# Kernel tuning notes

Measured on AMD Instinct MI355X. Metric: run time of the kernel, lower is better.

## Reference

```python
import jax, jax.numpy as jnp
import numpy as np

N_QUBITS = 13
DEPTH = 4
DIM = 2 ** N_QUBITS
PI = 3.141592653589793

# qubit 0 = most significant bit of the basis-state index
_idx = np.arange(DIM)
BITS = np.stack([(_idx >> (N_QUBITS - 1 - q)) & 1 for q in range(N_QUBITS)], axis=1)  # (DIM, n)
SIGNS = jnp.asarray(1.0 - 2.0 * BITS, dtype=jnp.float32)                               # Z eigenvalues, (DIM, n)
PARITY = jnp.asarray((-1.0) ** BITS.sum(axis=1), dtype=jnp.float32)                    # <Z^{(x)n}> diagonal, (DIM,)
# CZ entangling chain (q, q+1): diagonal (-1)^{sum_q b_q b_{q+1}}
ENT = jnp.asarray((-1.0) ** (BITS[:, :-1] * BITS[:, 1:]).sum(axis=1), dtype=jnp.float32)


def fwht(psi):
    """Normalized fast Walsh-Hadamard transform (H on every qubit), psi: (B, DIM) complex."""
    B = psi.shape[0]
    for q in range(N_QUBITS):
        psi = psi.reshape(B, 2 ** q, 2, -1)
        psi = jnp.stack([psi[:, :, 0] + psi[:, :, 1], psi[:, :, 0] - psi[:, :, 1]], axis=2)
    return psi.reshape(B, DIM) * (2.0 ** (-N_QUBITS / 2))


def feature_map_state(x):
    """Havlicek ZZ feature map: psi = D(x) H^n D(x) H^n |0...0>.
    Diagonal phase per basis state b: sum_j x_j s_j(b) + sum_{j<k} (pi-x_j)(pi-x_k) s_j(b) s_k(b)."""
    a = PI - x                                              # (B, n)
    u = x @ SIGNS.T                                         # (B, DIM)
    v = a @ SIGNS.T                                         # (B, DIM)
    phi = u + 0.5 * (v * v - jnp.sum(a * a, axis=1, keepdims=True))  # pair term via (sum)^2 trick
    d = jnp.exp(1j * phi)                                   # complex64 diagonal
    psi = jnp.full((x.shape[0], DIM), DIM ** -0.5, dtype=jnp.complex64)  # H^n |0>
    psi = fwht(d * psi)
    return d * psi


def _apply_1q(psi, U, q):
    """Apply 2x2 complex gate U to qubit q (bit-sliced)."""
    B = psi.shape[0]
    psi = psi.reshape(B, 2 ** q, 2, -1)
    a0, a1 = psi[:, :, 0], psi[:, :, 1]
    out = jnp.stack([U[0, 0] * a0 + U[0, 1] * a1, U[1, 0] * a0 + U[1, 1] * a1], axis=2)
    return out.reshape(B, DIM)


def variational_apply(psi, theta):
    """(DEPTH+1) layers of per-qubit Rz(b)Ry(a), CZ-chain entanglers between layers."""
    th = theta.reshape(DEPTH + 1, N_QUBITS, 2)
    for l in range(DEPTH + 1):
        if l > 0:
            psi = psi * ENT
        for q in range(N_QUBITS):
            ca = jnp.cos(0.5 * th[l, q, 0])
            sa = jnp.sin(0.5 * th[l, q, 0])
            em = jnp.exp(-0.5j * th[l, q, 1])
            ep = jnp.exp(0.5j * th[l, q, 1])
            U = jnp.stack([jnp.stack([em * ca, -em * sa]), jnp.stack([ep * sa, ep * ca])])
            psi = _apply_1q(psi, U, q)
    return psi


def setup_inputs() -> dict:
    key = jax.random.key(0)
    k1, k2 = jax.random.split(key)
    x = jax.random.normal(k1, (512, N_QUBITS), dtype=jnp.float32)
    theta = 0.1 * jax.random.normal(k2, ((DEPTH + 1) * N_QUBITS * 2,), dtype=jnp.float32)
    bias = jnp.zeros((1,), dtype=jnp.float32)
    return {"x": x, "theta": theta, "bias": bias}


def reference(x, theta, bias):
    psi = feature_map_state(x)
    psi = variational_apply(psi, theta)
    prob = psi.real ** 2 + psi.imag ** 2              # (B, DIM)
    logit = prob @ PARITY + bias[0]                   # (B,)
    return jnp.stack([-logit, logit], axis=1)         # two-class logits
```

## Files before the change

kernel.cpp:

```cpp
#include <hip/hip_runtime.h>
#include <hip/hip_fp16.h>

#define NQ   13
#define DIM  8192
#define PI_F 3.14159265358979323846f
#define NT   256
#define NAMP 32

#define NSLOT 9216

__device__ __forceinline__ int baseH(int t) { return 36 * t; }
__device__ __forceinline__ int baseL(int t) {
  int c = ((t & 1) << 7) | ((t & 2) << 5) | (t >> 2);
  return c + 4 * (c >> 5);
}

union F4H { float4 f; __half2 h[4]; };

__device__ __forceinline__ void rsincos(float x, float* s, float* c) {
  const float INV2PI = 0.15915494309189535f;
  const float TWOPI  = 6.283185307179586f;
  float r = x * INV2PI;
  r -= rintf(r);
  float ang = r * TWOPI;
  *s = __sinf(ang);
  *c = __cosf(ang);
}

__device__ __forceinline__ float2 f2add(float2 a, float2 b) {
  return make_float2(a.x + b.x, a.y + b.y);
}
__device__ __forceinline__ float2 f2sub(float2 a, float2 b) {
  return make_float2(a.x - b.x, a.y - b.y);
}
__device__ __forceinline__ float2 cphase(float2 v, float cs, float sn) {
  return make_float2(fmaf(cs, v.x, -sn * v.y), fmaf(cs, v.y, sn * v.x));
}
__device__ __forceinline__ float2 cmul(float2 a, float2 b) {
  return make_float2(fmaf(a.x, b.x, -a.y * b.y), fmaf(a.x, b.y, a.y * b.x));
}

template<int MASK>
__device__ __forceinline__ __half2 xorLaneH(__half2 v) {
  union { __half2 h; int i; } u, r; u.h = v;
  if constexpr (MASK == 1)
    r.i = __builtin_amdgcn_update_dpp(u.i, u.i, 0xB1, 0xF, 0xF, false);
  else
    r.i = __builtin_amdgcn_update_dpp(u.i, u.i, 0x4E, 0xF, 0xF, false);
  return r.h;
}

__device__ __forceinline__ void loadHh(const __half2* __restrict__ sAmp, int t, __half2* amp) {
  const __half2* p = sAmp + baseH(t);
  #pragma unroll
  for (int k = 0; k < 8; k++) {
    F4H u; u.f = *reinterpret_cast<const float4*>(p + 4 * k);
    #pragma unroll
    for (int c = 0; c < 4; c++) amp[4 * k + c] = u.h[c];
  }
}
__device__ __forceinline__ void storeHh(__half2* __restrict__ sAmp, int t, const __half2* amp) {
  __half2* p = sAmp + baseH(t);
  #pragma unroll
  for (int k = 0; k < 8; k++) {
    F4H u;
    #pragma unroll
    for (int c = 0; c < 4; c++) u.h[c] = amp[4 * k + c];
    *reinterpret_cast<float4*>(p + 4 * k) = u.f;
  }
}
__device__ __forceinline__ void loadLh(const __half2* __restrict__ sAmp, int t, __half2* amp) {
  const __half2* p = sAmp + baseL(t);
  #pragma unroll
  for (int j = 0; j < NAMP; j++) amp[j] = p[288 * j];
}
__device__ __forceinline__ void storeLh(__half2* __restrict__ sAmp, int t, const __half2* amp) {
  __half2* p = sAmp + baseL(t);
  #pragma unroll
  for (int j = 0; j < NAMP; j++) p[288 * j] = amp[j];
}

template<int KB>
__device__ __forceinline__ void fwht_bit(float2* amp) {
  #pragma unroll
  for (int j = 0; j < NAMP; j++) if (!(j & (1 << KB))) {
    int j1 = j | (1 << KB);
    float2 a0 = amp[j], a1 = amp[j1];
    amp[j]  = f2add(a0, a1);
    amp[j1] = f2sub(a0, a1);
  }
}
template<int KB>
__device__ __forceinline__ void fwht_bitH(__half2* amp) {
  #pragma unroll
  for (int j = 0; j < NAMP; j++) if (!(j & (1 << KB))) {
    int j1 = j | (1 << KB);
    __half2 a0 = amp[j], a1 = amp[j1];
    amp[j]  = __hadd2(a0, a1);
    amp[j1] = __hsub2(a0, a1);
  }
}
template<int KB>
__device__ __forceinline__ void applyRyH(__half2* amp, __half2 nta, __half2 sa) {
  #pragma unroll
  for (int j = 0; j < NAMP; j++) if (!(j & (1 << KB))) {
    int j1 = j | (1 << KB);
    amp[j]  = __hfma2(nta, amp[j1], amp[j]);
    amp[j1] = __hfma2(sa,  amp[j],  amp[j1]);
    amp[j]  = __hfma2(nta, amp[j1], amp[j]);
  }
}
template<int MASK>
__device__ __forceinline__ void laneRyH(__half2* amp, __half2 c2, __half2 spm) {
  #pragma unroll
  for (int j = 0; j < NAMP; j++) {
    __half2 p = xorLaneH<MASK>(amp[j]);
    amp[j] = __hfma2(spm, p, __hmul2(c2, amp[j]));
  }
}
template<int MASK>
__device__ __forceinline__ void laneFwhtH(__half2* amp, __half2 sgn) {
  #pragma unroll
  for (int j = 0; j < NAMP; j++) {
    __half2 p = xorLaneH<MASK>(amp[j]);
    amp[j] = __hfma2(sgn, amp[j], p);
  }
}

template<int PAT>
__device__ __forceinline__ void buildTree(const float* __restrict__ w, float bias,
                                          int t, float* s) {
  float base = bias;
  if constexpr (PAT == 0) {
    #pragma unroll
    for (int k = 0; k < 8; k++) base += ((t >> k) & 1) ? w[5 + k] : 0.0f;
  } else {
    constexpr int BM[8] = {7, 6, 0, 1, 2, 3, 4, 5};
    #pragma unroll
    for (int k = 0; k < 8; k++) base += ((t >> k) & 1) ? w[BM[k]] : 0.0f;
  }
  s[0] = base;
  #pragma unroll
  for (int k = 0; k < 5; k++) {
    float wp = w[(PAT == 0) ? k : 8 + k];
    #pragma unroll
    for (int m = 0; m < (1 << k); m++) s[m | (1 << k)] = s[m] + wp;
  }
}

template<int PAT, bool INIT>
__device__ __forceinline__ void featureDiag(float2* amp,
                                            const float* __restrict__ wXp,
                                            const float* __restrict__ wAp,
                                            const float* __restrict__ consp, int t) {
  float u[NAMP], v[NAMP];
  buildTree<PAT>(wXp, consp[0], t, u);
  buildTree<PAT>(wAp, consp[1], t, v);
  float A2 = consp[2];
  #pragma unroll
  for (int j = 0; j < NAMP; j++) {
    float phi = u[j] + 0.5f * (v[j] * v[j] - A2);
    float sn, cs; rsincos(phi, &sn, &cs);
    if constexpr (INIT) amp[j] = make_float2(cs, sn);
    else                amp[j] = cphase(amp[j], cs, sn);
  }
}

__device__ __forceinline__ void applyDiagH(float2* amp,
                                           const float* __restrict__ wb,
                                           const float* __restrict__ eR,
                                           const float* __restrict__ eI,
                                           float bias, int t) {
  float base = bias;
  #pragma unroll
  for (int k = 0; k < 8; k++) base += ((t >> k) & 1) ? wb[5 + k] : 0.0f;
  float2 c[16];
  { float sn, cs; rsincos(base, &sn, &cs);
    float sg = (__popc(t & (t >> 1)) & 1) ? -1.0f : 1.0f;
    c[0] = make_float2(cs * sg, sn * sg); }
  #pragma unroll
  for (int k = 0; k < 4; k++) {
    float2 ep = make_float2(eR[k], eI[k]);
    float2 em = make_float2(-ep.x, -ep.y);
    #pragma unroll
    for (int m = 0; m < (1 << k); m++) {
      bool neg = (k >= 1) && ((m >> (k - 1)) & 1);
      c[m | (1 << k)] = cmul(c[m], neg ? em : ep);
    }
  }
  #pragma unroll
  for (int j = 0; j < 16; j++) amp[j] = cphase(amp[j], c[j].x, c[j].y);
  float2 e4 = make_float2(eR[4], eI[4]);
  if (t & 1) { e4.x = -e4.x; e4.y = -e4.y; }
  float2 e4m = make_float2(-e4.x, -e4.y);
  #pragma unroll
  for (int j = 16; j < 32; j++) {
    float2 cc = cmul(c[j - 16], ((j >> 3) & 1) ? e4m : e4);
    amp[j] = cphase(amp[j], cc.x, cc.y);
  }
}

__device__ __forceinline__ void applyDiagL(float2* amp,
                                           const float* __restrict__ wb,
                                           const float* __restrict__ eR,
                                           const float* __restrict__ eI,
                                           float bias, int t) {
  constexpr int BM[8] = {7, 6, 0, 1, 2, 3, 4, 5};
  float base = bias;
  #pragma unroll
  for (int k = 0; k < 8; k++) base += ((t >> k) & 1) ? wb[BM[k]] : 0.0f;
  const int ci = ((t & 1) << 7) | ((t & 2) << 5) | (t >> 2);
  float2 c[16];
  { float sn, cs; rsincos(base, &sn, &cs);
    float sg = (__popc(ci & (ci >> 1)) & 1) ? -1.0f : 1.0f;
    c[0] = make_float2(cs * sg, sn * sg); }
  {
    float2 e0 = make_float2(eR[8], eI[8]);
    if (t & 1) { e0.x = -e0.x; e0.y = -e0.y; }
    c[1] = cmul(c[0], e0);
  }
  #pragma unroll
  for (int k = 1; k < 4; k++) {
    float2 ep = make_float2(eR[8 + k], eI[8 + k]);
    float2 em = make_float2(-ep.x, -ep.y);
    #pragma unroll
    for (int m = 0; m < (1 << k); m++)
      c[m | (1 << k)] = cmul(c[m], ((m >> (k - 1)) & 1) ? em : ep);
  }
  #pragma unroll
  for (int j = 0; j < 16; j++) amp[j] = cphase(amp[j], c[j].x, c[j].y);
  float2 e4 = make_float2(eR[12], eI[12]);
  float2 e4m = make_float2(-e4.x, -e4.y);
  #pragma unroll
  for (int j = 16; j < 32; j++) {
    float2 cc = cmul(c[j - 16], ((j >> 3) & 1) ? e4m : e4);
    amp[j] = cphase(amp[j], cc.x, cc.y);
  }
}

__device__ __forceinline__ void gatesH(__half2* ampH,
                                       const __half2* __restrict__ hNTA,
                                       const __half2* __restrict__ hSA,
                                       const __half2* __restrict__ hC2,
                                       const __half2* __restrict__ hS2,
                                       int g0, int lane) {
  { __half2 s2 = hS2[g0 + 7]; laneRyH<1>(ampH, hC2[g0 + 7], (lane & 1) ? s2 : __hneg2(s2)); }
  { __half2 s2 = hS2[g0 + 6]; laneRyH<2>(ampH, hC2[g0 + 6], (lane & 2) ? s2 : __hneg2(s2)); }
  applyRyH<0>(ampH, hNTA[g0 + 12], hSA[g0 + 12]);
  applyRyH<1>(ampH, hNTA[g0 + 11], hSA[g0 + 11]);
  applyRyH<2>(ampH, hNTA[g0 + 10], hSA[g0 + 10]);
  applyRyH<3>(ampH, hNTA[g0 + 9],  hSA[g0 + 9]);
  applyRyH<4>(ampH, hNTA[g0 + 8],  hSA[g0 + 8]);
}
__device__ __forceinline__ void gatesL(__half2* ampH,
                                       const __half2* __restrict__ hNTA,
                                       const __half2* __restrict__ hSA,
                                       const __half2* __restrict__ hC2,
                                       const __half2* __restrict__ hS2,
                                       int g0, int lane) {
  { __half2 s2 = hS2[g0 + 5]; laneRyH<1>(ampH, hC2[g0 + 5], (lane & 1) ? s2 : __hneg2(s2)); }
  applyRyH<0>(ampH, hNTA[g0 + 4], hSA[g0 + 4]);
  applyRyH<1>(ampH, hNTA[g0 + 3], hSA[g0 + 3]);
  applyRyH<2>(ampH, hNTA[g0 + 2], hSA[g0 + 2]);
  applyRyH<3>(ampH, hNTA[g0 + 1], hSA[g0 + 1]);
  applyRyH<4>(ampH, hNTA[g0 + 0], hSA[g0 + 0]);
}

__global__ __launch_bounds__(NT, 1) void qc_kernel(
    const float* __restrict__ xin,
    const float* __restrict__ thin,
    const float* __restrict__ bin,
    float* __restrict__ out) {
  __shared__ alignas(16) __half2 sAmp[NSLOT];
  __shared__ __half2 hNTA[65], hSA[65];
  __shared__ __half2 hC2[65], hS2[65];
  __shared__ float gBbit[65];
  __shared__ float eBr[65], eBi[65];
  __shared__ float wX[13], wA[13];
  __shared__ float cons[8];
  __shared__ float red[NT / 64];

  const int t = threadIdx.x;
  const int lane = t & 63;
  const int b = blockIdx.x;

  if (t < NQ) {
    float xq = xin[b * NQ + t];
    float aq = PI_F - xq;
    wX[12 - t] = -2.0f * xq;
    wA[12 - t] = -2.0f * aq;
  }
  if (t < 65) {
    float av = thin[2 * t];
    float bv = thin[2 * t + 1];
    float ca = cosf(0.5f * av);
    float sa = sinf(0.5f * av);
    float ta = sa / (1.0f + ca);
    hNTA[t] = __float2half2_rn(-ta);
    hSA[t]  = __float2half2_rn(sa);
    hC2[t]  = __float2half2_rn(ca);
    hS2[t]  = __float2half2_rn(sa);
    int l = t / NQ, q = t % NQ;
    int s = l * NQ + (12 - q);
    gBbit[s] = bv;
    eBr[s] = cosf(bv);
    eBi[s] = sinf(bv);
  }
  __syncthreads();
  if (t == 0) {
    float X = 0.f, A = 0.f, A2 = 0.f;
    for (int p = 0; p < NQ; p++) {
      float xq = -0.5f * wX[p], aq = -0.5f * wA[p];
      X += xq; A += aq; A2 += aq * aq;
    }
    cons[0] = X; cons[1] = A; cons[2] = A2;
    for (int l = 0; l < 5; l++) {
      float s = 0.f;
      for (int p = 0; p < NQ; p++) s += gBbit[l * NQ + p];
      cons[3 + l] = -0.5f * s;
    }
  }
  __syncthreads();

  const __half2 P1 = __float2half2_rn(1.0f), M1 = __float2half2_rn(-1.0f);

  {
    float2 ampF[NAMP];
    featureDiag<0, true>(ampF, wX, wA, cons, t);
    fwht_bit<0>(ampF); fwht_bit<1>(ampF); fwht_bit<2>(ampF);
    fwht_bit<3>(ampF); fwht_bit<4>(ampF);
    __half2 ampH[NAMP];
    #pragma unroll
    for (int j = 0; j < NAMP; j++) ampH[j] = __float22half2_rn(ampF[j]);
    laneFwhtH<1>(ampH, (lane & 1) ? M1 : P1);
    laneFwhtH<2>(ampH, (lane & 2) ? M1 : P1);
    storeHh(sAmp, t, ampH);
  }
  __syncthreads();

  {
    __half2 ampH[NAMP];
    loadLh(sAmp, t, ampH);
    laneFwhtH<1>(ampH, (lane & 1) ? M1 : P1);
    fwht_bitH<0>(ampH); fwht_bitH<1>(ampH); fwht_bitH<2>(ampH);
    fwht_bitH<3>(ampH); fwht_bitH<4>(ampH);
    float2 ampF[NAMP];
    #pragma unroll
    for (int j = 0; j < NAMP; j++) ampF[j] = __half22float2(ampH[j]);
    featureDiag<1, false>(ampF, wX, wA, cons, t);
    #pragma unroll
    for (int j = 0; j < NAMP; j++) ampH[j] = __float22half2_rn(ampF[j]);
    gatesL(ampH, hNTA, hSA, hC2, hS2, 0, lane);
    storeLh(sAmp, t, ampH);
  }
  __syncthreads();

  for (int l = 0; l < 4; l += 2) {
    const int ga = l * NQ, gb = ga + NQ, gc = gb + NQ;
    {
      __half2 ampH[NAMP];
      loadHh(sAmp, t, ampH);
      gatesH(ampH, hNTA, hSA, hC2, hS2, ga, lane);
      float2 ampF[NAMP];
      #pragma unroll
      for (int j = 0; j < NAMP; j++) ampF[j] = __half22float2(ampH[j]);
      applyDiagH(ampF, gBbit + ga, eBr + ga, eBi + ga, cons[3 + l], t);
      #pragma unroll
      for (int j = 0; j < NAMP; j++) ampH[j] = __float22half2_rn(ampF[j]);
      gatesH(ampH, hNTA, hSA, hC2, hS2, gb, lane);
      storeHh(sAmp, t, ampH);
    }
    __syncthreads();
    {
      __half2 ampH[NAMP];
      loadLh(sAmp, t, ampH);
      gatesL(ampH, hNTA, hSA, hC2, hS2, gb, lane);
      float2 ampF[NAMP];
      #pragma unroll
      for (int j = 0; j < NAMP; j++) ampF[j] = __half22float2(ampH[j]);
      applyDiagL(ampF, gBbit + gb, eBr + gb, eBi + gb, cons[3 + l + 1], t);
      #pragma unroll
      for (int j = 0; j < NAMP; j++) ampH[j] = __float22half2_rn(ampF[j]);
      gatesL(ampH, hNTA, hSA, hC2, hS2, gc, lane);
      storeLh(sAmp, t, ampH);
    }
    __syncthreads();
  }

  float acc = 0.0f;
  {
    const int ga = 4 * NQ;
    __half2 ampH[NAMP];
    loadHh(sAmp, t, ampH);
    gatesH(ampH, hNTA, hSA, hC2, hS2, ga, lane);
    int pt = __popc(t) & 1;
    #pragma unroll
    for (int j = 0; j < NAMP; j++) {
      float2 a = __half22float2(ampH[j]);
      float p2 = fmaf(a.x, a.x, a.y * a.y);
      acc += ((pt + __popc(j)) & 1) ? -p2 : p2;
    }
  }

  #pragma unroll
  for (int off = 32; off > 0; off >>= 1) acc += __shfl_down(acc, off, 64);
  if ((t & 63) == 0) red[t >> 6] = acc;
  __syncthreads();
  if (t == 0) {
    float total = red[0] + red[1] + red[2] + red[3];
    float logit = total * (1.0f / 67108864.0f) + bin[0];
    out[b * 2 + 0] = -logit;
    out[b * 2 + 1] = logit;
  }
}

extern "C" void kernel_launch(void* const* d_in, const int* in_sizes, int n_in,
                              void* d_out, int out_size, void* d_ws, size_t ws_size,
                              hipStream_t stream) {
  const float* x  = (const float*)d_in[0];
  const float* th = (const float*)d_in[1];
  const float* bi = (const float*)d_in[2];
  float* out = (float*)d_out;
  int B = in_sizes[0] / NQ;
  qc_kernel<<<B, NT, 0, stream>>>(x, th, bi, out);
}
```

Baseline: 88.41 us.

## Keep state in registers with lane shuffles and pairwise wave exchanges instead of transposes

Replaces the alternating high/low shared-memory transposes with a fixed layout. Each thread keeps 32 amplitudes in registers, lane-level qubits are handled with DPP or shfl_xor, and the two wave-level qubits are handled by pairwise exchanges through shared memory. Diagonal phases are now computed on half2 amplitudes with per-element float conversion. This removes the strided transposed shared-memory loads, but it adds more syncthreads per layer (two exchanges each with two barriers) and uses ds_swizzle/shfl for the masks 4, 16 and 32.

```diff
diff --git a/kernel.cpp b/kernel.cpp
--- a/kernel.cpp
+++ b/kernel.cpp
@@ -7,13 +7,8 @@
 #define NT   256
 #define NAMP 32
 
+__device__ __forceinline__ int base0(int t) { return 36 * t; }
 #define NSLOT 9216
-
-__device__ __forceinline__ int baseH(int t) { return 36 * t; }
-__device__ __forceinline__ int baseL(int t) {
-  int c = ((t & 1) << 7) | ((t & 2) << 5) | (t >> 2);
-  return c + 4 * (c >> 5);
-}
 
 union F4H { float4 f; __half2 h[4]; };
 
@@ -27,12 +22,6 @@
   *c = __cosf(ang);
 }
 
-__device__ __forceinline__ float2 f2add(float2 a, float2 b) {
-  return make_float2(a.x + b.x, a.y + b.y);
-}
-__device__ __forceinline__ float2 f2sub(float2 a, float2 b) {
-  return make_float2(a.x - b.x, a.y - b.y);
-}
 __device__ __forceinline__ float2 cphase(float2 v, float cs, float sn) {
   return make_float2(fmaf(cs, v.x, -sn * v.y), fmaf(cs, v.y, sn * v.x));
 }
@@ -41,17 +30,21 @@
 }
 
 template<int MASK>
-__device__ __forceinline__ __half2 xorLaneH(__half2 v) {
+__device__ __forceinline__ __half2 lanePartner(__half2 v) {
   union { __half2 h; int i; } u, r; u.h = v;
   if constexpr (MASK == 1)
     r.i = __builtin_amdgcn_update_dpp(u.i, u.i, 0xB1, 0xF, 0xF, false);
+  else if constexpr (MASK == 2)
+    r.i = __builtin_amdgcn_update_dpp(u.i, u.i, 0x4E, 0xF, 0xF, false);
+  else if constexpr (MASK == 8)
+    r.i = __builtin_amdgcn_update_dpp(u.i, u.i, 0x128, 0xF, 0xF, false);
   else
-    r.i = __builtin_amdgcn_update_dpp(u.i, u.i, 0x4E, 0xF, 0xF, false);
+    r.i = __shfl_xor(u.i, MASK, 64);
   return r.h;
 }
 
-__device__ __forceinline__ void loadHh(const __half2* __restrict__ sAmp, int t, __half2* amp) {
-  const __half2* p = sAmp + baseH(t);
+__device__ __forceinline__ void loadXh(const __half2* __restrict__ sAmp, int t, __half2* amp) {
+  const __half2* p = sAmp + base0(t);
   #pragma unroll
   for (int k = 0; k < 8; k++) {
     F4H u; u.f = *reinterpret_cast<const float4*>(p + 4 * k);
@@ -59,8 +52,8 @@
     for (int c = 0; c < 4; c++) amp[4 * k + c] = u.h[c];
   }
 }
-__device__ __forceinline__ void storeHh(__half2* __restrict__ sAmp, int t, const __half2* amp) {
-  __half2* p = sAmp + baseH(t);
+__device__ __forceinline__ void storeXh(__half2* __restrict__ sAmp, int t, const __half2* amp) {
+  __half2* p = sAmp + base0(t);
   #pragma unroll
   for (int k = 0; k < 8; k++) {
     F4H u;
@@ -69,27 +62,7 @@
     *reinterpret_cast<float4*>(p + 4 * k) = u.f;
   }
 }
-__device__ __forceinline__ void loadLh(const __half2* __restrict__ sAmp, int t, __half2* amp) {
-  const __half2* p = sAmp + baseL(t);
-  #pragma unroll
-  for (int j = 0; j < NAMP; j++) amp[j] = p[288 * j];
-}
-__device__ __forceinline__ void storeLh(__half2* __restrict__ sAmp, int t, const __half2* amp) {
-  __half2* p = sAmp + baseL(t);
-  #pragma unroll
-  for (int j = 0; j < NAMP; j++) p[288 * j] = amp[j];
-}
-
-template<int KB>
-__device__ __forceinline__ void fwht_bit(float2* amp) {
-  #pragma unroll
-  for (int j = 0; j < NAMP; j++) if (!(j & (1 << KB))) {
-    int j1 = j | (1 << KB);
-    float2 a0 = amp[j], a1 = amp[j1];
-    amp[j]  = f2add(a0, a1);
-    amp[j1] = f2sub(a0, a1);
-  }
-}
+
 template<int KB>
 __device__ __forceinline__ void fwht_bitH(__half2* amp) {
   #pragma unroll
@@ -114,7 +87,7 @@
 __device__ __forceinline__ void laneRyH(__half2* amp, __half2 c2, __half2 spm) {
   #pragma unroll
   for (int j = 0; j < NAMP; j++) {
-    __half2 p = xorLaneH<MASK>(amp[j]);
+    __half2 p = lanePartner<MASK>(amp[j]);
     amp[j] = __hfma2(spm, p, __hmul2(c2, amp[j]));
   }
 }
@@ -122,103 +95,67 @@
 __device__ __forceinline__ void laneFwhtH(__half2* amp, __half2 sgn) {
   #pragma unroll
   for (int j = 0; j < NAMP; j++) {
-    __half2 p = xorLaneH<MASK>(amp[j]);
+    __half2 p = lanePartner<MASK>(amp[j]);
     amp[j] = __hfma2(sgn, amp[j], p);
   }
 }
 
-template<int PAT>
-__device__ __forceinline__ void buildTree(const float* __restrict__ w, float bias,
-                                          int t, float* s) {
-  float base = bias;
-  if constexpr (PAT == 0) {
-    #pragma unroll
-    for (int k = 0; k < 8; k++) base += ((t >> k) & 1) ? w[5 + k] : 0.0f;
-  } else {
-    constexpr int BM[8] = {7, 6, 0, 1, 2, 3, 4, 5};
-    #pragma unroll
-    for (int k = 0; k < 8; k++) base += ((t >> k) & 1) ? w[BM[k]] : 0.0f;
-  }
-  s[0] = base;
-  #pragma unroll
-  for (int k = 0; k < 5; k++) {
-    float wp = w[(PAT == 0) ? k : 8 + k];
-    #pragma unroll
-    for (int m = 0; m < (1 << k); m++) s[m | (1 << k)] = s[m] + wp;
-  }
-}
-
-template<int PAT, bool INIT>
-__device__ __forceinline__ void featureDiag(float2* amp,
+template<bool INIT>
+__device__ __forceinline__ void featureDiag(__half2* amp,
                                             const float* __restrict__ wXp,
                                             const float* __restrict__ wAp,
-                                            const float* __restrict__ consp, int t) {
-  float u[NAMP], v[NAMP];
-  buildTree<PAT>(wXp, consp[0], t, u);
-  buildTree<PAT>(wAp, consp[1], t, v);
-  float A2 = consp[2];
+                                            const float* __restrict__ consp,
+                                            int tl, int w0, int w1) {
+  float u16[16], v16[16];
+  float ub = consp[0], vb = consp[1];
+  #pragma unroll
+  for (int k = 0; k < 6; k++) if ((tl >> k) & 1) { ub += wXp[k]; vb += wAp[k]; }
+  if (w0) { ub += wXp[6]; vb += wAp[6]; }
+  if (w1) { ub += wXp[7]; vb += wAp[7]; }
+  u16[0] = ub; v16[0] = vb;
+  #pragma unroll
+  for (int k = 0; k < 4; k++) {
+    float wu = wXp[8 + k], wv = wAp[8 + k];
+    #pragma unroll
+    for (int m = 0; m < (1 << k); m++) {
+      u16[m | (1 << k)] = u16[m] + wu;
+      v16[m | (1 << k)] = v16[m] + wv;
+    }
+  }
+  const float du = wXp[12], dv = wAp[12], A2 = consp[2];
   #pragma unroll
   for (int j = 0; j < NAMP; j++) {
-    float phi = u[j] + 0.5f * (v[j] * v[j] - A2);
+    float uu = u16[j & 15] + ((j >> 4) ? du : 0.0f);
+    float vv = v16[j & 15] + ((j >> 4) ? dv : 0.0f);
+    float phi = uu + 0.5f * (vv * vv - A2);
     float sn, cs; rsincos(phi, &sn, &cs);
-    if constexpr (INIT) amp[j] = make_float2(cs, sn);
-    else                amp[j] = cphase(amp[j], cs, sn);
-  }
-}
-
-__device__ __forceinline__ void applyDiagH(float2* amp,
-                                           const float* __restrict__ wb,
-                                           const float* __restrict__ eR,
-                                           const float* __restrict__ eI,
-                                           float bias, int t) {
+    if constexpr (INIT) {
+      amp[j] = __float22half2_rn(make_float2(cs, sn));
+    } else {
+      float2 a = __half22float2(amp[j]);
+      amp[j] = __float22half2_rn(cphase(a, cs, sn));
+    }
+  }
+}
+
+__device__ __forceinline__ void applyDiag(__half2* amp,
+                                          const float* __restrict__ wb,
+                                          const float* __restrict__ eR,
+                                          const float* __restrict__ eI,
+                                          float bias, int tl, int w0, int w1) {
   float base = bias;
   #pragma unroll
-  for (int k = 0; k < 8; k++) base += ((t >> k) & 1) ? wb[5 + k] : 0.0f;
+  for (int k = 0; k < 6; k++) if ((tl >> k) & 1) base += wb[k];
+  if (w0) base += wb[6];
+  if (w1) base += wb[7];
   float2 c[16];
   { float sn, cs; rsincos(base, &sn, &cs);
-    float sg = (__popc(t & (t >> 1)) & 1) ? -1.0f : 1.0f;
-    c[0] = make_float2(cs * sg, sn * sg); }
-  #pragma unroll
-  for (int k = 0; k < 4; k++) {
-    float2 ep = make_float2(eR[k], eI[k]);
-    float2 em = make_float2(-ep.x, -ep.y);
-    #pragma unroll
-    for (int m = 0; m < (1 << k); m++) {
-      bool neg = (k >= 1) && ((m >> (k - 1)) & 1);
-      c[m | (1 << k)] = cmul(c[m], neg ? em : ep);
-    }
-  }
-  #pragma unroll
-  for (int j = 0; j < 16; j++) amp[j] = cphase(amp[j], c[j].x, c[j].y);
-  float2 e4 = make_float2(eR[4], eI[4]);
-  if (t & 1) { e4.x = -e4.x; e4.y = -e4.y; }
-  float2 e4m = make_float2(-e4.x, -e4.y);
-  #pragma unroll
-  for (int j = 16; j < 32; j++) {
-    float2 cc = cmul(c[j - 16], ((j >> 3) & 1) ? e4m : e4);
-    amp[j] = cphase(amp[j], cc.x, cc.y);
-  }
-}
-
-__device__ __forceinline__ void applyDiagL(float2* amp,
-                                           const float* __restrict__ wb,
-                                           const float* __restrict__ eR,
-                                           const float* __restrict__ eI,
-                                           float bias, int t) {
-  constexpr int BM[8] = {7, 6, 0, 1, 2, 3, 4, 5};
-  float base = bias;
-  #pragma unroll
-  for (int k = 0; k < 8; k++) base += ((t >> k) & 1) ? wb[BM[k]] : 0.0f;
-  const int ci = ((t & 1) << 7) | ((t & 2) << 5) | (t >> 2);
-  float2 c[16];
-  { float sn, cs; rsincos(base, &sn, &cs);
-    float sg = (__popc(ci & (ci >> 1)) & 1) ? -1.0f : 1.0f;
-    c[0] = make_float2(cs * sg, sn * sg); }
-  {
-    float2 e0 = make_float2(eR[8], eI[8]);
-    if (t & 1) { e0.x = -e0.x; e0.y = -e0.y; }
-    c[1] = cmul(c[0], e0);
-  }
+    int sg = (__popc(tl & (tl >> 1)) ^ (((tl >> 5) & 1) & w0) ^ (w0 & w1)) & 1;
+    float s = sg ? -1.0f : 1.0f;
+    c[0] = make_float2(cs * s, sn * s); }
+  { float2 e0 = make_float2(eR[8], eI[8]);
+    if (w1) { e0.x = -e0.x; e0.y = -e0.y; }
+    c[1] = cmul(c[0], e0); }
   #pragma unroll
   for (int k = 1; k < 4; k++) {
     float2 ep = make_float2(eR[8 + k], eI[8 + k]);
@@ -228,42 +165,18 @@
       c[m | (1 << k)] = cmul(c[m], ((m >> (k - 1)) & 1) ? em : ep);
   }
   #pragma unroll
-  for (int j = 0; j < 16; j++) amp[j] = cphase(amp[j], c[j].x, c[j].y);
-  float2 e4 = make_float2(eR[12], eI[12]);
+  for (int j = 0; j < 16; j++) {
+    float2 a = __half22float2(amp[j]);
+    amp[j] = __float22half2_rn(cphase(a, c[j].x, c[j].y));
+  }
+  float2 e4  = make_float2(eR[12], eI[12]);
   float2 e4m = make_float2(-e4.x, -e4.y);
   #pragma unroll
   for (int j = 16; j < 32; j++) {
-    float2 cc = cmul(c[j - 16], ((j >> 3) & 1) ? e4m : e4);
-    amp[j] = cphase(amp[j], cc.x, cc.y);
-  }
-}
-
-__device__ __forceinline__ void gatesH(__half2* ampH,
-                                       const __half2* __restrict__ hNTA,
-                                       const __half2* __restrict__ hSA,
-                                       const __half2* __restrict__ hC2,
-                                       const __half2* __restrict__ hS2,
-                                       int g0, int lane) {
-  { __half2 s2 = hS2[g0 + 7]; laneRyH<1>(ampH, hC2[g0 + 7], (lane & 1) ? s2 : __hneg2(s2)); }
-  { __half2 s2 = hS2[g0 + 6]; laneRyH<2>(ampH, hC2[g0 + 6], (lane & 2) ? s2 : __hneg2(s2)); }
-  applyRyH<0>(ampH, hNTA[g0 + 12], hSA[g0 + 12]);
-  applyRyH<1>(ampH, hNTA[g0 + 11], hSA[g0 + 11]);
-  applyRyH<2>(ampH, hNTA[g0 + 10], hSA[g0 + 10]);
-  applyRyH<3>(ampH, hNTA[g0 + 9],  hSA[g0 + 9]);
-  applyRyH<4>(ampH, hNTA[g0 + 8],  hSA[g0 + 8]);
-}
-__device__ __forceinline__ void gatesL(__half2* ampH,
-                                       const __half2* __restrict__ hNTA,
-                                       const __half2* __restrict__ hSA,
-                                       const __half2* __restrict__ hC2,
-                                       const __half2* __restrict__ hS2,
-                                       int g0, int lane) {
-  { __half2 s2 = hS2[g0 + 5]; laneRyH<1>(ampH, hC2[g0 + 5], (lane & 1) ? s2 : __hneg2(s2)); }
-  applyRyH<0>(ampH, hNTA[g0 + 4], hSA[g0 + 4]);
-  applyRyH<1>(ampH, hNTA[g0 + 3], hSA[g0 + 3]);
-  applyRyH<2>(ampH, hNTA[g0 + 2], hSA[g0 + 2]);
-  applyRyH<3>(ampH, hNTA[g0 + 1], hSA[g0 + 1]);
-  applyRyH<4>(ampH, hNTA[g0 + 0], hSA[g0 + 0]);
+    float2 cc = cmul(c[j - 16], (((j - 16) >> 3) & 1) ? e4m : e4);
+    float2 a = __half22float2(amp[j]);
+    amp[j] = __float22half2_rn(cphase(a, cc.x, cc.y));
+  }
 }
 
 __global__ __launch_bounds__(NT, 1) void qc_kernel(
@@ -271,7 +184,7 @@
     const float* __restrict__ thin,
     const float* __restrict__ bin,
     float* __restrict__ out) {
-  __shared__ alignas(16) __half2 sAmp[NSLOT];
+  __shared__ alignas(16) __half2 sEx[NSLOT];
   __shared__ __half2 hNTA[65], hSA[65];
   __shared__ __half2 hC2[65], hS2[65];
   __shared__ float gBbit[65];
@@ -280,9 +193,11 @@
   __shared__ float cons[8];
   __shared__ float red[NT / 64];
 
-  const int t = threadIdx.x;
-  const int lane = t & 63;
-  const int b = blockIdx.x;
+  const int t  = threadIdx.x;
+  const int tl = t & 63;
+  const int w0 = (t >> 6) & 1;
+  const int w1 = (t >> 7) & 1;
+  const int b  = blockIdx.x;
 
   if (t < NQ) {
     float xq = xin[b * NQ + t];
@@ -322,83 +237,75 @@
   }
   __syncthreads();
 
+  __half2 amp[NAMP];
   const __half2 P1 = __float2half2_rn(1.0f), M1 = __float2half2_rn(-1.0f);
 
-  {
-    float2 ampF[NAMP];
-    featureDiag<0, true>(ampF, wX, wA, cons, t);
-    fwht_bit<0>(ampF); fwht_bit<1>(ampF); fwht_bit<2>(ampF);
-    fwht_bit<3>(ampF); fwht_bit<4>(ampF);
-    __half2 ampH[NAMP];
-    #pragma unroll
-    for (int j = 0; j < NAMP; j++) ampH[j] = __float22half2_rn(ampF[j]);
-    laneFwhtH<1>(ampH, (lane & 1) ? M1 : P1);
-    laneFwhtH<2>(ampH, (lane & 2) ? M1 : P1);
-    storeHh(sAmp, t, ampH);
-  }
-  __syncthreads();
-
-  {
-    __half2 ampH[NAMP];
-    loadLh(sAmp, t, ampH);
-    laneFwhtH<1>(ampH, (lane & 1) ? M1 : P1);
-    fwht_bitH<0>(ampH); fwht_bitH<1>(ampH); fwht_bitH<2>(ampH);
-    fwht_bitH<3>(ampH); fwht_bitH<4>(ampH);
-    float2 ampF[NAMP];
-    #pragma unroll
-    for (int j = 0; j < NAMP; j++) ampF[j] = __half22float2(ampH[j]);
-    featureDiag<1, false>(ampF, wX, wA, cons, t);
-    #pragma unroll
-    for (int j = 0; j < NAMP; j++) ampH[j] = __float22half2_rn(ampF[j]);
-    gatesL(ampH, hNTA, hSA, hC2, hS2, 0, lane);
-    storeLh(sAmp, t, ampH);
-  }
-  __syncthreads();
-
-  for (int l = 0; l < 4; l += 2) {
-    const int ga = l * NQ, gb = ga + NQ, gc = gb + NQ;
-    {
-      __half2 ampH[NAMP];
-      loadHh(sAmp, t, ampH);
-      gatesH(ampH, hNTA, hSA, hC2, hS2, ga, lane);
-      float2 ampF[NAMP];
+  auto exchFwht = [&](int bit) {
+    __syncthreads();
+    storeXh(sEx, t, amp);
+    __syncthreads();
+    __half2 p[NAMP];
+    loadXh(sEx, t ^ (64 << bit), p);
+    int wb = bit ? w1 : w0;
+    __half2 sgn = wb ? M1 : P1;
+    #pragma unroll
+    for (int j = 0; j < NAMP; j++) amp[j] = __hfma2(sgn, amp[j], p[j]);
+  };
+  auto exchRy = [&](int bit, int gq) {
+    __syncthreads();
+    storeXh(sEx, t, amp);
+    __syncthreads();
+    __half2 p[NAMP];
+    loadXh(sEx, t ^ (64 << bit), p);
+    int wb = bit ? w1 : w0;
+    __half2 c2 = hC2[gq], s2 = hS2[gq];
+    __half2 spm = wb ? s2 : __hneg2(s2);
+    #pragma unroll
+    for (int j = 0; j < NAMP; j++)
+      amp[j] = __hfma2(spm, p[j], __hmul2(c2, amp[j]));
+  };
+
+  featureDiag<true>(amp, wX, wA, cons, tl, w0, w1);
+
+  fwht_bitH<0>(amp); fwht_bitH<1>(amp); fwht_bitH<2>(amp);
+  fwht_bitH<3>(amp); fwht_bitH<4>(amp);
+  laneFwhtH<1>(amp,  (tl & 1)  ? M1 : P1);
+  laneFwhtH<2>(amp,  (tl & 2)  ? M1 : P1);
+  laneFwhtH<4>(amp,  (tl & 4)  ? M1 : P1);
+  laneFwhtH<8>(amp,  (tl & 8)  ? M1 : P1);
+  laneFwhtH<16>(amp, (tl & 16) ? M1 : P1);
+  laneFwhtH<32>(amp, (tl & 32) ? M1 : P1);
+  exchFwht(0);
+  exchFwht(1);
+
+  featureDiag<false>(amp, wX, wA, cons, tl, w0, w1);
+
+  float acc = 0.0f;
+  for (int l = 0; l < 5; ++l) {
+    const int g = l * NQ;
+    applyRyH<4>(amp, hNTA[g + 0], hSA[g + 0]);
+    applyRyH<3>(amp, hNTA[g + 1], hSA[g + 1]);
+    applyRyH<2>(amp, hNTA[g + 2], hSA[g + 2]);
+    applyRyH<1>(amp, hNTA[g + 3], hSA[g + 3]);
+    applyRyH<0>(amp, hNTA[g + 4], hSA[g + 4]);
+    { __half2 s2 = hS2[g + 12]; laneRyH<1>(amp,  hC2[g + 12], (tl & 1)  ? s2 : __hneg2(s2)); }
+    { __half2 s2 = hS2[g + 11]; laneRyH<2>(amp,  hC2[g + 11], (tl & 2)  ? s2 : __hneg2(s2)); }
+    { __half2 s2 = hS2[g + 10]; laneRyH<4>(amp,  hC2[g + 10], (tl & 4)  ? s2 : __hneg2(s2)); }
+    { __half2 s2 = hS2[g + 9];  laneRyH<8>(amp,  hC2[g + 9],  (tl & 8)  ? s2 : __hneg2(s2)); }
+    { __half2 s2 = hS2[g + 8];  laneRyH<16>(amp, hC2[g + 8],  (tl & 16) ? s2 : __hneg2(s2)); }
+    { __half2 s2 = hS2[g + 7];  laneRyH<32>(amp, hC2[g + 7],  (tl & 32) ? s2 : __hneg2(s2)); }
+    exchRy(0, g + 6);
+    exchRy(1, g + 5);
+    if (l < 4) {
+      applyDiag(amp, gBbit + g, eBr + g, eBi + g, cons[3 + l], tl, w0, w1);
+    } else {
+      int pt = __popc(t) & 1;
       #pragma unroll
-      for (int j = 0; j < NAMP; j++) ampF[j] = __half22float2(ampH[j]);
-      applyDiagH(ampF, gBbit + ga, eBr + ga, eBi + ga, cons[3 + l], t);
-      #pragma unroll
-      for (int j = 0; j < NAMP; j++) ampH[j] = __float22half2_rn(ampF[j]);
-      gatesH(ampH, hNTA, hSA, hC2, hS2, gb, lane);
-      storeHh(sAmp, t, ampH);
-    }
-    __syncthreads();
-    {
-      __half2 ampH[NAMP];
-      loadLh(sAmp, t, ampH);
-      gatesL(ampH, hNTA, hSA, hC2, hS2, gb, lane);
-      float2 ampF[NAMP];
-      #pragma unroll
-      for (int j = 0; j < NAMP; j++) ampF[j] = __half22float2(ampH[j]);
-      applyDiagL(ampF, gBbit + gb, eBr + gb, eBi + gb, cons[3 + l + 1], t);
-      #pragma unroll
-      for (int j = 0; j < NAMP; j++) ampH[j] = __float22half2_rn(ampF[j]);
-      gatesL(ampH, hNTA, hSA, hC2, hS2, gc, lane);
-      storeLh(sAmp, t, ampH);
-    }
-    __syncthreads();
-  }
-
-  float acc = 0.0f;
-  {
-    const int ga = 4 * NQ;
-    __half2 ampH[NAMP];
-    loadHh(sAmp, t, ampH);
-    gatesH(ampH, hNTA, hSA, hC2, hS2, ga, lane);
-    int pt = __popc(t) & 1;
-    #pragma unroll
-    for (int j = 0; j < NAMP; j++) {
-      float2 a = __half22float2(ampH[j]);
-      float p2 = fmaf(a.x, a.x, a.y * a.y);
-      acc += ((pt + __popc(j)) & 1) ? -p2 : p2;
+      for (int j = 0; j < NAMP; j++) {
+        float2 a = __half22float2(amp[j]);
+        float p2 = fmaf(a.x, a.x, a.y * a.y);
+        acc += ((pt + __popc(j)) & 1) ? -p2 : p2;
+      }
     }
   }
 
```

Result: slower. 98.81 us (+11.8%).

## Remap the second-phase shared-memory layout to vectorized column loads with extra lane shuffles

Applied to the files above, without the earlier changes.

The qubit-to-register/lane mapping for the second (L/C) phase is changed so each thread loads 4 consecutive half2 amplitudes with float4 accesses (8 vector loads) instead of 32 scalar strided loads. To make this work, more qubits are handled through cross-lane exchanges: DPP row_ror for mask 8 and __shfl_xor for masks 4 and 16 in the first FWHT stage, plus an extra lane Ry in the H phase. The feature and entangler diagonal generators are rewritten for the new bit mapping. The aim is to cut LDS instruction count and bank-conflict cost, in exchange for extra cross-lane shuffle work (ds_bpermute for the non-DPP masks).

```diff
diff --git a/kernel.cpp b/kernel.cpp
--- a/kernel.cpp
+++ b/kernel.cpp
@@ -6,13 +6,12 @@
 #define PI_F 3.14159265358979323846f
 #define NT   256
 #define NAMP 32
-
 #define NSLOT 9216
 
 __device__ __forceinline__ int baseH(int t) { return 36 * t; }
-__device__ __forceinline__ int baseL(int t) {
-  int c = ((t & 1) << 7) | ((t & 2) << 5) | (t >> 2);
-  return c + 4 * (c >> 5);
+__device__ __forceinline__ int fC(int t) {
+  return ((t & 1) << 7) | (((t >> 1) & 1) << 9) | (((t >> 2) & 0x1F) << 2)
+       | (((t >> 7) & 1) << 8);
 }
 
 union F4H { float4 f; __half2 h[4]; };
@@ -41,12 +40,16 @@
 }
 
 template<int MASK>
-__device__ __forceinline__ __half2 xorLaneH(__half2 v) {
+__device__ __forceinline__ __half2 lanePartner(__half2 v) {
   union { __half2 h; int i; } u, r; u.h = v;
   if constexpr (MASK == 1)
     r.i = __builtin_amdgcn_update_dpp(u.i, u.i, 0xB1, 0xF, 0xF, false);
+  else if constexpr (MASK == 2)
+    r.i = __builtin_amdgcn_update_dpp(u.i, u.i, 0x4E, 0xF, 0xF, false);
+  else if constexpr (MASK == 8)
+    r.i = __builtin_amdgcn_update_dpp(u.i, u.i, 0x128, 0xF, 0xF, false);
   else
-    r.i = __builtin_amdgcn_update_dpp(u.i, u.i, 0x4E, 0xF, 0xF, false);
+    r.i = __shfl_xor(u.i, MASK, 64);
   return r.h;
 }
 
@@ -69,15 +72,24 @@
     *reinterpret_cast<float4*>(p + 4 * k) = u.f;
   }
 }
-__device__ __forceinline__ void loadLh(const __half2* __restrict__ sAmp, int t, __half2* amp) {
-  const __half2* p = sAmp + baseL(t);
-  #pragma unroll
-  for (int j = 0; j < NAMP; j++) amp[j] = p[288 * j];
-}
-__device__ __forceinline__ void storeLh(__half2* __restrict__ sAmp, int t, const __half2* amp) {
-  __half2* p = sAmp + baseL(t);
-  #pragma unroll
-  for (int j = 0; j < NAMP; j++) p[288 * j] = amp[j];
+__device__ __forceinline__ void loadCh(const __half2* __restrict__ sAmp, int cpad, __half2* amp) {
+  const __half2* p = sAmp + cpad;
+  #pragma unroll
+  for (int g = 0; g < 8; g++) {
+    F4H u; u.f = *reinterpret_cast<const float4*>(p + 1152 * g);
+    #pragma unroll
+    for (int c = 0; c < 4; c++) amp[4 * g + c] = u.h[c];
+  }
+}
+__device__ __forceinline__ void storeCh(__half2* __restrict__ sAmp, int cpad, const __half2* amp) {
+  __half2* p = sAmp + cpad;
+  #pragma unroll
+  for (int g = 0; g < 8; g++) {
+    F4H u;
+    #pragma unroll
+    for (int c = 0; c < 4; c++) u.h[c] = amp[4 * g + c];
+    *reinterpret_cast<float4*>(p + 1152 * g) = u.f;
+  }
 }
 
 template<int KB>
@@ -114,7 +126,7 @@
 __device__ __forceinline__ void laneRyH(__half2* amp, __half2 c2, __half2 spm) {
   #pragma unroll
   for (int j = 0; j < NAMP; j++) {
-    __half2 p = xorLaneH<MASK>(amp[j]);
+    __half2 p = lanePartner<MASK>(amp[j]);
     amp[j] = __hfma2(spm, p, __hmul2(c2, amp[j]));
   }
 }
@@ -122,40 +134,30 @@
 __device__ __forceinline__ void laneFwhtH(__half2* amp, __half2 sgn) {
   #pragma unroll
   for (int j = 0; j < NAMP; j++) {
-    __half2 p = xorLaneH<MASK>(amp[j]);
+    __half2 p = lanePartner<MASK>(amp[j]);
     amp[j] = __hfma2(sgn, amp[j], p);
   }
 }
 
-template<int PAT>
-__device__ __forceinline__ void buildTree(const float* __restrict__ w, float bias,
-                                          int t, float* s) {
-  float base = bias;
-  if constexpr (PAT == 0) {
-    #pragma unroll
-    for (int k = 0; k < 8; k++) base += ((t >> k) & 1) ? w[5 + k] : 0.0f;
-  } else {
-    constexpr int BM[8] = {7, 6, 0, 1, 2, 3, 4, 5};
-    #pragma unroll
-    for (int k = 0; k < 8; k++) base += ((t >> k) & 1) ? w[BM[k]] : 0.0f;
-  }
-  s[0] = base;
+template<bool INIT>
+__device__ __forceinline__ void featureDiagH(float2* amp,
+                                             const float* __restrict__ wXp,
+                                             const float* __restrict__ wAp,
+                                             const float* __restrict__ consp, int t) {
+  float u[NAMP], v[NAMP];
+  float ub = consp[0], vb = consp[1];
+  #pragma unroll
+  for (int k = 0; k < 8; k++) if ((t >> k) & 1) { ub += wXp[5 + k]; vb += wAp[5 + k]; }
+  u[0] = ub; v[0] = vb;
   #pragma unroll
   for (int k = 0; k < 5; k++) {
-    float wp = w[(PAT == 0) ? k : 8 + k];
-    #pragma unroll
-    for (int m = 0; m < (1 << k); m++) s[m | (1 << k)] = s[m] + wp;
-  }
-}
-
-template<int PAT, bool INIT>
-__device__ __forceinline__ void featureDiag(float2* amp,
-                                            const float* __restrict__ wXp,
-                                            const float* __restrict__ wAp,
-                                            const float* __restrict__ consp, int t) {
-  float u[NAMP], v[NAMP];
-  buildTree<PAT>(wXp, consp[0], t, u);
-  buildTree<PAT>(wAp, consp[1], t, v);
+    float wu = wXp[k], wv = wAp[k];
+    #pragma unroll
+    for (int m = 0; m < (1 << k); m++) {
+      u[m | (1 << k)] = u[m] + wu;
+      v[m | (1 << k)] = v[m] + wv;
+    }
+  }
   float A2 = consp[2];
   #pragma unroll
   for (int j = 0; j < NAMP; j++) {
@@ -163,6 +165,34 @@
     float sn, cs; rsincos(phi, &sn, &cs);
     if constexpr (INIT) amp[j] = make_float2(cs, sn);
     else                amp[j] = cphase(amp[j], cs, sn);
+  }
+}
+
+__device__ __forceinline__ void featureDiagC(float2* amp,
+                                             const float* __restrict__ wXp,
+                                             const float* __restrict__ wAp,
+                                             const float* __restrict__ consp, int ic) {
+  float u[NAMP], v[NAMP];
+  float ub = consp[0], vb = consp[1];
+  #pragma unroll
+  for (int k = 2; k <= 9; k++) if ((ic >> k) & 1) { ub += wXp[k]; vb += wAp[k]; }
+  u[0] = ub; v[0] = vb;
+  constexpr int P[5] = {0, 1, 10, 11, 12};
+  #pragma unroll
+  for (int k = 0; k < 5; k++) {
+    float wu = wXp[P[k]], wv = wAp[P[k]];
+    #pragma unroll
+    for (int m = 0; m < (1 << k); m++) {
+      u[m | (1 << k)] = u[m] + wu;
+      v[m | (1 << k)] = v[m] + wv;
+    }
+  }
+  float A2 = consp[2];
+  #pragma unroll
+  for (int j = 0; j < NAMP; j++) {
+    float phi = u[j] + 0.5f * (v[j] * v[j] - A2);
+    float sn, cs; rsincos(phi, &sn, &cs);
+    amp[j] = cphase(amp[j], cs, sn);
   }
 }
 
@@ -200,36 +230,37 @@
   }
 }
 
-__device__ __forceinline__ void applyDiagL(float2* amp,
+__device__ __forceinline__ void applyDiagC(float2* amp,
                                            const float* __restrict__ wb,
                                            const float* __restrict__ eR,
                                            const float* __restrict__ eI,
-                                           float bias, int t) {
-  constexpr int BM[8] = {7, 6, 0, 1, 2, 3, 4, 5};
+                                           float bias, int ic) {
   float base = bias;
   #pragma unroll
-  for (int k = 0; k < 8; k++) base += ((t >> k) & 1) ? wb[BM[k]] : 0.0f;
-  const int ci = ((t & 1) << 7) | ((t & 2) << 5) | (t >> 2);
+  for (int k = 2; k <= 9; k++) base += ((ic >> k) & 1) ? wb[k] : 0.0f;
   float2 c[16];
   { float sn, cs; rsincos(base, &sn, &cs);
-    float sg = (__popc(ci & (ci >> 1)) & 1) ? -1.0f : 1.0f;
+    float sg = (__popc(ic & (ic >> 1)) & 1) ? -1.0f : 1.0f;
     c[0] = make_float2(cs * sg, sn * sg); }
-  {
-    float2 e0 = make_float2(eR[8], eI[8]);
-    if (t & 1) { e0.x = -e0.x; e0.y = -e0.y; }
-    c[1] = cmul(c[0], e0);
-  }
-  #pragma unroll
-  for (int k = 1; k < 4; k++) {
-    float2 ep = make_float2(eR[8 + k], eI[8 + k]);
-    float2 em = make_float2(-ep.x, -ep.y);
-    #pragma unroll
-    for (int m = 0; m < (1 << k); m++)
-      c[m | (1 << k)] = cmul(c[m], ((m >> (k - 1)) & 1) ? em : ep);
-  }
+  { float2 e0 = make_float2(eR[0], eI[0]);
+    c[1] = cmul(c[0], e0); }
+  { float2 e1 = make_float2(eR[1], eI[1]);
+    if ((ic >> 2) & 1) { e1.x = -e1.x; e1.y = -e1.y; }
+    float2 e1m = make_float2(-e1.x, -e1.y);
+    c[2] = cmul(c[0], e1);
+    c[3] = cmul(c[1], e1m); }
+  { float2 e2 = make_float2(eR[10], eI[10]);
+    if ((ic >> 9) & 1) { e2.x = -e2.x; e2.y = -e2.y; }
+    #pragma unroll
+    for (int m = 0; m < 4; m++) c[m | 4] = cmul(c[m], e2); }
+  { float2 e3 = make_float2(eR[11], eI[11]);
+    float2 e3m = make_float2(-e3.x, -e3.y);
+    #pragma unroll
+    for (int m = 0; m < 8; m++)
+      c[m | 8] = cmul(c[m], ((m >> 2) & 1) ? e3m : e3); }
   #pragma unroll
   for (int j = 0; j < 16; j++) amp[j] = cphase(amp[j], c[j].x, c[j].y);
-  float2 e4 = make_float2(eR[12], eI[12]);
+  float2 e4  = make_float2(eR[12], eI[12]);
   float2 e4m = make_float2(-e4.x, -e4.y);
   #pragma unroll
   for (int j = 16; j < 32; j++) {
@@ -246,21 +277,21 @@
                                        int g0, int lane) {
   { __half2 s2 = hS2[g0 + 7]; laneRyH<1>(ampH, hC2[g0 + 7], (lane & 1) ? s2 : __hneg2(s2)); }
   { __half2 s2 = hS2[g0 + 6]; laneRyH<2>(ampH, hC2[g0 + 6], (lane & 2) ? s2 : __hneg2(s2)); }
+  { __half2 s2 = hS2[g0 + 4]; laneRyH<8>(ampH, hC2[g0 + 4], (lane & 8) ? s2 : __hneg2(s2)); }
   applyRyH<0>(ampH, hNTA[g0 + 12], hSA[g0 + 12]);
   applyRyH<1>(ampH, hNTA[g0 + 11], hSA[g0 + 11]);
   applyRyH<2>(ampH, hNTA[g0 + 10], hSA[g0 + 10]);
   applyRyH<3>(ampH, hNTA[g0 + 9],  hSA[g0 + 9]);
   applyRyH<4>(ampH, hNTA[g0 + 8],  hSA[g0 + 8]);
 }
-__device__ __forceinline__ void gatesL(__half2* ampH,
+__device__ __forceinline__ void gatesC(__half2* ampH,
                                        const __half2* __restrict__ hNTA,
                                        const __half2* __restrict__ hSA,
                                        const __half2* __restrict__ hC2,
                                        const __half2* __restrict__ hS2,
                                        int g0, int lane) {
   { __half2 s2 = hS2[g0 + 5]; laneRyH<1>(ampH, hC2[g0 + 5], (lane & 1) ? s2 : __hneg2(s2)); }
-  applyRyH<0>(ampH, hNTA[g0 + 4], hSA[g0 + 4]);
-  applyRyH<1>(ampH, hNTA[g0 + 3], hSA[g0 + 3]);
+  { __half2 s2 = hS2[g0 + 3]; laneRyH<2>(ampH, hC2[g0 + 3], (lane & 2) ? s2 : __hneg2(s2)); }
   applyRyH<2>(ampH, hNTA[g0 + 2], hSA[g0 + 2]);
   applyRyH<3>(ampH, hNTA[g0 + 1], hSA[g0 + 1]);
   applyRyH<4>(ampH, hNTA[g0 + 0], hSA[g0 + 0]);
@@ -282,6 +313,8 @@
 
   const int t = threadIdx.x;
   const int lane = t & 63;
+  const int ic = fC(t);
+  const int cpad = ic + 4 * (ic >> 5);
   const int b = blockIdx.x;
 
   if (t < NQ) {
@@ -326,32 +359,33 @@
 
   {
     float2 ampF[NAMP];
-    featureDiag<0, true>(ampF, wX, wA, cons, t);
+    featureDiagH<true>(ampF, wX, wA, cons, t);
     fwht_bit<0>(ampF); fwht_bit<1>(ampF); fwht_bit<2>(ampF);
     fwht_bit<3>(ampF); fwht_bit<4>(ampF);
     __half2 ampH[NAMP];
     #pragma unroll
     for (int j = 0; j < NAMP; j++) ampH[j] = __float22half2_rn(ampF[j]);
-    laneFwhtH<1>(ampH, (lane & 1) ? M1 : P1);
-    laneFwhtH<2>(ampH, (lane & 2) ? M1 : P1);
+    laneFwhtH<1>(ampH,  (lane & 1)  ? M1 : P1);
+    laneFwhtH<2>(ampH,  (lane & 2)  ? M1 : P1);
+    laneFwhtH<8>(ampH,  (lane & 8)  ? M1 : P1);
+    laneFwhtH<4>(ampH,  (lane & 4)  ? M1 : P1);
+    laneFwhtH<16>(ampH, (lane & 16) ? M1 : P1);
     storeHh(sAmp, t, ampH);
   }
   __syncthreads();
 
   {
     __half2 ampH[NAMP];
-    loadLh(sAmp, t, ampH);
-    laneFwhtH<1>(ampH, (lane & 1) ? M1 : P1);
-    fwht_bitH<0>(ampH); fwht_bitH<1>(ampH); fwht_bitH<2>(ampH);
-    fwht_bitH<3>(ampH); fwht_bitH<4>(ampH);
+    loadCh(sAmp, cpad, ampH);
+    fwht_bitH<2>(ampH); fwht_bitH<3>(ampH); fwht_bitH<4>(ampH);
     float2 ampF[NAMP];
     #pragma unroll
     for (int j = 0; j < NAMP; j++) ampF[j] = __half22float2(ampH[j]);
-    featureDiag<1, false>(ampF, wX, wA, cons, t);
+    featureDiagC(ampF, wX, wA, cons, ic);
     #pragma unroll
     for (int j = 0; j < NAMP; j++) ampH[j] = __float22half2_rn(ampF[j]);
-    gatesL(ampH, hNTA, hSA, hC2, hS2, 0, lane);
-    storeLh(sAmp, t, ampH);
+    gatesC(ampH, hNTA, hSA, hC2, hS2, 0, lane);
+    storeCh(sAmp, cpad, ampH);
   }
   __syncthreads();
 
@@ -373,16 +407,16 @@
     __syncthreads();
     {
       __half2 ampH[NAMP];
-      loadLh(sAmp, t, ampH);
-      gatesL(ampH, hNTA, hSA, hC2, hS2, gb, lane);
+      loadCh(sAmp, cpad, ampH);
+      gatesC(ampH, hNTA, hSA, hC2, hS2, gb, lane);
       float2 ampF[NAMP];
       #pragma unroll
       for (int j = 0; j < NAMP; j++) ampF[j] = __half22float2(ampH[j]);
-      applyDiagL(ampF, gBbit + gb, eBr + gb, eBi + gb, cons[3 + l + 1], t);
+      applyDiagC(ampF, gBbit + gb, eBr + gb, eBi + gb, cons[3 + l + 1], ic);
       #pragma unroll
       for (int j = 0; j < NAMP; j++) ampH[j] = __float22half2_rn(ampF[j]);
-      gatesL(ampH, hNTA, hSA, hC2, hS2, gc, lane);
-      storeLh(sAmp, t, ampH);
+      gatesC(ampH, hNTA, hSA, hC2, hS2, gc, lane);
+      storeCh(sAmp, cpad, ampH);
     }
     __syncthreads();
   }
```

New measurement: 90.31 us. 1.02x slower.
